# Optimization experiments

Hardware: AMD Instinct MI355X
Metric: run time of the kernel (lower is better)

## Reference

```python
import jax, jax.numpy as jnp
import numpy as np

N_POINTS = 10000
N_SHAPES = 100
N_RAYS = 4096
SH_COEFFS = 16  # (sh_degree+1)^2, degree 3


def sh_basis(d):
    """Degree-3 real SH basis. d: [B,3] normalized dirs -> [B,16]."""
    x, y, z = d[:, 0], d[:, 1], d[:, 2]
    one = jnp.ones_like(x)
    return jnp.stack([
        0.282095 * one,
        0.488603 * y, 0.488603 * z, 0.488603 * x,
        1.092548 * x * y, 1.092548 * y * z, 0.315392 * (3.0 * z * z - 1.0),
        1.092548 * x * z, 0.546274 * (x * x - y * y),
        0.590044 * y * (3.0 * x * x - y * y), 2.890611 * x * y * z,
        0.457046 * y * (5.0 * z * z - 1.0), 0.373176 * z * (5.0 * z * z - 3.0),
        0.457046 * x * (5.0 * z * z - 1.0), 1.445306 * z * (x * x - y * y),
        0.590044 * x * (x * x - 3.0 * y * y),
    ], axis=-1)


def setup_inputs() -> dict:
    key = jax.random.key(0)
    ks = jax.random.split(key, 7)
    return {
        "rays_o": jax.random.normal(ks[0], (N_RAYS, 3), jnp.float32),
        "rays_d": jax.random.normal(ks[1], (N_RAYS, 3), jnp.float32),
        "positions": jax.random.normal(ks[2], (N_POINTS, 3), jnp.float32),
        "shape_indices": jax.random.randint(ks[3], (N_POINTS,), 0, N_SHAPES, jnp.int32),
        "log_delta": jax.random.normal(ks[4], (N_SHAPES,), jnp.float32) * 0.1 - 1.0,
        "log_sigma": jax.random.normal(ks[5], (N_SHAPES,), jnp.float32) * 0.1,
        "raw_opacity": jax.random.uniform(ks[6], (N_POINTS,), jnp.float32, -0.1, 0.1),
        "sh_coeffs": jax.random.normal(jax.random.fold_in(key, 7), (N_POINTS, SH_COEFFS, 3), jnp.float32) * 0.1,
    }


def reference(rays_o, rays_d, positions, shape_indices, log_delta, log_sigma, raw_opacity, sh_coeffs):
    # normalize view directions (F.normalize)
    d_norm = rays_d / jnp.linalg.norm(rays_d, axis=-1, keepdims=True)

    opacity = jax.nn.sigmoid(raw_opacity)           # [N]
    point_delta = jnp.exp(log_delta)[shape_indices]  # [N]
    point_sigma = jnp.exp(log_sigma)[shape_indices]  # [N]

    # SH shading: colors [N, B, 3]
    sh = sh_basis(d_norm)                            # [B, 16]
    colors = jax.nn.sigmoid(jnp.einsum('nkc,bk->nbc', sh_coeffs, sh))

    # per point / per ray geometry
    rel = positions[:, None, :] - rays_o[None, :, :]   # [N, B, 3]
    dist = jnp.linalg.norm(rel, axis=2)                # [N, B]
    dirs = rel / (dist[..., None] + 1e-8)              # [N, B, 3]
    dot = jnp.sum(dirs * d_norm[None, :, :], axis=2)   # [N, B]

    contrib = (jnp.exp(-point_delta[:, None] * (1.0 - dot) ** 2)
               * point_sigma[:, None] * opacity[:, None] / (dist + 1e-6))  # [N, B]
    total = jnp.sum(contrib, axis=0, keepdims=True)
    w = contrib / (total + 1e-8)                       # [N, B]

    rgb = jnp.sum(colors * w[..., None], axis=0)       # [B, 3]
    depth = jnp.sum(dist * w, axis=0)[:, None]         # [B, 1]
    opac = jnp.broadcast_to(jnp.mean(opacity), (rgb.shape[0],))
    return rgb, depth, opac
```

## Files before the change

### kernel.cpp

```cpp
#include <hip/hip_runtime.h>
#include <hip/hip_bf16.h>

#define NPTS    10000
#define NRAYS   4096
#define PTILES  640
#define RTILES  256
#define RGROUPS 64
#define PCHUNKS 16
#define TPC     (PTILES / PCHUNKS)
#define ABLK    64
#define BBLK    160
#define LOG2E   1.44269504f

typedef float f4  __attribute__((ext_vector_type(4)));
typedef short s8v __attribute__((ext_vector_type(8)));

__device__ s8v   g_A[RTILES * 3 * 64];
__device__ s8v   g_B[PTILES * 5 * 64];
__device__ float g_acc[NRAYS * 5];
__device__ float g_oppart[BBLK];

__device__ __forceinline__ float fast_rcp(float x)  { return __builtin_amdgcn_rcpf(x); }
__device__ __forceinline__ float fast_exp2(float x) { return __builtin_amdgcn_exp2f(x); }
__device__ __forceinline__ float fast_sigmoid(float x) { return fast_rcp(1.0f + fast_exp2(-x * LOG2E)); }

__device__ __forceinline__ unsigned short bf16r(float x) {
    __hip_bfloat16 h = __float2bfloat16(x);
    return *reinterpret_cast<unsigned short*>(&h);
}
__device__ __forceinline__ float bf16f(unsigned short u) {
    return __uint_as_float((unsigned)u << 16);
}
__device__ __forceinline__ float bfhi(float x) { return bf16f(bf16r(x)); }

__device__ __forceinline__ s8v pk8(float a, float b, float c, float d,
                                   float e, float f, float g, float h) {
    s8v r;
    r[0] = (short)bf16r(a); r[1] = (short)bf16r(b);
    r[2] = (short)bf16r(c); r[3] = (short)bf16r(d);
    r[4] = (short)bf16r(e); r[5] = (short)bf16r(f);
    r[6] = (short)bf16r(g); r[7] = (short)bf16r(h);
    return r;
}

template <int CTRL>
__device__ __forceinline__ float dpp_step(float x) {
    return x + __int_as_float(
        __builtin_amdgcn_update_dpp(0, __float_as_int(x), CTRL, 0xf, 0xf, true));
}
__device__ __forceinline__ float rowsum15(float x) {
    x = dpp_step<0x111>(x);
    x = dpp_step<0x112>(x);
    x = dpp_step<0x114>(x);
    x = dpp_step<0x118>(x);
    return x;
}

__global__ __launch_bounds__(256) void setup(const float* __restrict__ ro,
                                             const float* __restrict__ rd,
                                             const float* __restrict__ pos,
                                             const int*   __restrict__ sidx,
                                             const float* __restrict__ log_delta,
                                             const float* __restrict__ log_sigma,
                                             const float* __restrict__ raw_op,
                                             const float* __restrict__ shc) {
    s8v zero8 = pk8(0, 0, 0, 0, 0, 0, 0, 0);
    if (blockIdx.x < ABLK) {
        int t = blockIdx.x * 256 + threadIdx.x;
        int rt = t >> 6, lane = t & 63, quad = lane >> 4;
        int r = rt * 16 + (lane & 15);
        if (quad == 0) {
            float* a = g_acc + (size_t)r * 5;
            a[0] = a[1] = a[2] = a[3] = a[4] = 0.0f;
        }
        float ox = ro[r * 3 + 0], oy = ro[r * 3 + 1], oz = ro[r * 3 + 2];
        float rdx = rd[r * 3 + 0], rdy = rd[r * 3 + 1], rdz = rd[r * 3 + 2];
        float inv = __builtin_amdgcn_rsqf(rdx * rdx + rdy * rdy + rdz * rdz);
        float x = rdx * inv, y = rdy * inv, z = rdz * inv;
        float oo = ox * ox + oy * oy + oz * oz;
        float od = ox * x + oy * y + oz * z;
        float ohx = bfhi(ox), olx = ox - ohx;
        float ohy = bfhi(oy), oly = oy - ohy;
        float ohz = bfhi(oz), olz = oz - ohz;
        float dhx = bfhi(x),  dlx = x - dhx;
        float dhy = bfhi(y),  dly = y - dhy;
        float dhz = bfhi(z),  dlz = z - dhz;
        float ooh = bfhi(oo), ool = oo - ooh;
        float odh = bfhi(od), odl = od - odh;
        float zz = z * z, xx = x * x, yy = y * y;
        float sh[16];
        sh[0]  = LOG2E * 0.282095f;
        sh[1]  = LOG2E * 0.488603f * y;
        sh[2]  = LOG2E * 0.488603f * z;
        sh[3]  = LOG2E * 0.488603f * x;
        sh[4]  = LOG2E * 1.092548f * x * y;
        sh[5]  = LOG2E * 1.092548f * y * z;
        sh[6]  = LOG2E * 0.315392f * (3.0f * zz - 1.0f);
        sh[7]  = LOG2E * 1.092548f * x * z;
        sh[8]  = LOG2E * 0.546274f * (xx - yy);
        sh[9]  = LOG2E * 0.590044f * y * (3.0f * xx - yy);
        sh[10] = LOG2E * 2.890611f * x * y * z;
        sh[11] = LOG2E * 0.457046f * y * (5.0f * zz - 1.0f);
        sh[12] = LOG2E * 0.373176f * z * (5.0f * zz - 3.0f);
        sh[13] = LOG2E * 0.457046f * x * (5.0f * zz - 1.0f);
        sh[14] = LOG2E * 1.445306f * z * (xx - yy);
        sh[15] = LOG2E * 0.590044f * x * (xx - 3.0f * yy);

        s8v A0 = quad == 0 ? pk8(1, 1, ooh, ool, ohx, ohy, ohz, ohx)
               : quad == 1 ? pk8(ohy, ohz, olx, oly, olz, 0, 0, 0) : zero8;
        s8v A1 = quad == 0 ? pk8(dhx, dhy, dhz, dhx, dhy, dhz, dlx, dly)
               : quad == 1 ? pk8(dlz, odh, odl, 0, 0, 0, 0, 0) : zero8;
        s8v A2 = quad == 0 ? pk8(sh[0], sh[1], sh[2], sh[3], sh[4], sh[5], sh[6], sh[7])
               : quad == 1 ? pk8(sh[8], sh[9], sh[10], sh[11], sh[12], sh[13], sh[14], sh[15]) : zero8;
        s8v* pa = g_A + (size_t)rt * 3 * 64 + lane;
        pa[0 * 64] = A0; pa[1 * 64] = A1; pa[2 * 64] = A2;
    } else {
        int bb = blockIdx.x - ABLK;
        int t  = bb * 256 + threadIdx.x;
        int pt = t >> 6, lane = t & 63, quad = lane >> 4;
        int n  = pt * 16 + (lane & 15);
        float px, py, pz, w1, L0, op = 0.0f;
        float C0[16], C1[16], C2[16];
        if (n < NPTS) {
            px = pos[n * 3 + 0]; py = pos[n * 3 + 1]; pz = pos[n * 3 + 2];
            int s = sidx[n];
            op = fast_sigmoid(raw_op[n]);
            w1 = -__expf(log_delta[s]) * LOG2E;
            float w0 = __expf(log_sigma[s]) * op;
            L0 = __log2f(w0);
            const float* c = shc + (size_t)n * 48;
#pragma unroll
            for (int k = 0; k < 16; ++k) {
                C0[k] = c[k * 3 + 0]; C1[k] = c[k * 3 + 1]; C2[k] = c[k * 3 + 2];
            }
        } else {
            px = py = pz = 1e3f; w1 = 0.0f; L0 = -100.0f;
#pragma unroll
            for (int k = 0; k < 16; ++k) { C0[k] = 0; C1[k] = 0; C2[k] = 0; }
        }
        float pp  = px * px + py * py + pz * pz;
        float phx = bfhi(px), plx = px - phx;
        float phy = bfhi(py), ply = py - phy;
        float phz = bfhi(pz), plz = pz - phz;
        float pph = bfhi(pp), ppl = pp - pph;
        float w1h = bfhi(w1), w1l = w1 - w1h;
        float L0h = bfhi(L0), L0l = L0 - L0h;

        s8v B0 = quad == 0 ? pk8(pph, ppl, 1, 1, -2 * phx, -2 * phy, -2 * phz, -2 * plx)
               : quad == 1 ? pk8(-2 * ply, -2 * plz, -2 * phx, -2 * phy, -2 * phz, w1h, w1l, 0) : zero8;
        s8v B1 = quad == 0 ? pk8(phx, phy, phz, plx, ply, plz, phx, phy)
               : quad == 1 ? pk8(phz, -1, -1, L0h, L0l, 0, 0, 0) : zero8;
        s8v B2 = quad == 0 ? pk8(C0[0], C0[1], C0[2], C0[3], C0[4], C0[5], C0[6], C0[7])
               : quad == 1 ? pk8(C0[8], C0[9], C0[10], C0[11], C0[12], C0[13], C0[14], C0[15]) : zero8;
        s8v B3 = quad == 0 ? pk8(C1[0], C1[1], C1[2], C1[3], C1[4], C1[5], C1[6], C1[7])
               : quad == 1 ? pk8(C1[8], C1[9], C1[10], C1[11], C1[12], C1[13], C1[14], C1[15]) : zero8;
        s8v B4 = quad == 0 ? pk8(C2[0], C2[1], C2[2], C2[3], C2[4], C2[5], C2[6], C2[7])
               : quad == 1 ? pk8(C2[8], C2[9], C2[10], C2[11], C2[12], C2[13], C2[14], C2[15]) : zero8;
        s8v* pb = g_B + (size_t)pt * 5 * 64 + lane;
        pb[0 * 64] = B0; pb[1 * 64] = B1; pb[2 * 64] = B2; pb[3 * 64] = B3;
        pb[4 * 64] = B4;

        __shared__ float blk;
        if (threadIdx.x == 0) blk = 0.0f;
        __syncthreads();
        float v = (quad == 0) ? op : 0.0f;
#pragma unroll
        for (int off = 32; off > 0; off >>= 1) v += __shfl_down(v, off, 64);
        if ((threadIdx.x & 63) == 0) atomicAdd(&blk, v);
        __syncthreads();
        if (threadIdx.x == 0) g_oppart[bb] = blk;
    }
}

__global__ __launch_bounds__(256, 3) void nerf_main() {
    int rg = blockIdx.x & (RGROUPS - 1);
    int pc = blockIdx.x / RGROUPS;
    int wv = threadIdx.x >> 6, lane = threadIdx.x & 63;
    int rt = rg * 4 + wv;
    int quad = lane >> 4;

    const s8v* pa = g_A + (size_t)rt * 3 * 64 + lane;
    s8v a0 = pa[0 * 64], a1 = pa[1 * 64], a2 = pa[2 * 64];
    short one_bf = (short)0x3F80;
    s8v a4 = {0, 0, 0, 0, 0, 0, 0, 0};
    s8v a5 = {0, 0, 0, 0, 0, 0, 0, 0};
    if (quad == 1) { a4[5] = one_bf; a4[6] = one_bf; a5[3] = one_bf; a5[4] = one_bf; }
    f4 z = {0.0f, 0.0f, 0.0f, 0.0f};

    float acc[5][4];
#pragma unroll
    for (int v = 0; v < 5; ++v)
#pragma unroll
        for (int i = 0; i < 4; ++i) acc[v][i] = 0.0f;

    const s8v* pb = g_B + (size_t)(pc * TPC) * 5 * 64 + lane;
#pragma unroll 1
    for (int ti = 0; ti < TPC; ++ti, pb += 5 * 64) {
        s8v b0 = pb[0 * 64], b1 = pb[1 * 64], b2 = pb[2 * 64], b3 = pb[3 * 64];
        s8v b4 = pb[4 * 64];
        f4 c0 = __builtin_amdgcn_mfma_f32_16x16x32_bf16(a0, b0, z, 0, 0, 0);
        f4 c1 = __builtin_amdgcn_mfma_f32_16x16x32_bf16(a1, b1, z, 0, 0, 0);
        f4 c2 = __builtin_amdgcn_mfma_f32_16x16x32_bf16(a2, b2, z, 0, 0, 0);
        f4 c3 = __builtin_amdgcn_mfma_f32_16x16x32_bf16(a2, b3, z, 0, 0, 0);
        f4 c4 = __builtin_amdgcn_mfma_f32_16x16x32_bf16(a2, b4, z, 0, 0, 0);
        f4 c5 = __builtin_amdgcn_mfma_f32_16x16x32_bf16(a4, b0, z, 0, 0, 0);
        f4 c6 = __builtin_amdgcn_mfma_f32_16x16x32_bf16(a5, b1, z, 0, 0, 0);
#pragma unroll
        for (int i = 0; i < 4; ++i) {
            float d2  = c0[i], pd = c1[i];
            float inv = __builtin_amdgcn_rsqf(d2);
            float t   = 1.0f - pd * inv;
            float arg = fmaf(c5[i] * t, t, c6[i]);
            float contrib = fast_exp2(arg) * inv;
            float dist = d2 * inv;
            float e0 = 1.0f + fast_exp2(-c2[i]);
            float e1 = 1.0f + fast_exp2(-c3[i]);
            float e2 = 1.0f + fast_exp2(-c4[i]);
            float P  = e0 * e1, Pa = P * e2;
            float CI = contrib * fast_rcp(Pa);
            acc[0][i] = fmaf(CI, e1 * e2, acc[0][i]);
            acc[1][i] = fmaf(CI, e0 * e2, acc[1][i]);
            acc[2][i] = fmaf(CI, P, acc[2][i]);
            acc[3][i] = fmaf(dist, contrib, acc[3][i]);
            acc[4][i] += contrib;
        }
    }

#pragma unroll
    for (int v = 0; v < 5; ++v)
#pragma unroll
        for (int i = 0; i < 4; ++i) acc[v][i] = rowsum15(acc[v][i]);
    if ((lane & 15) == 15) {
#pragma unroll
        for (int i = 0; i < 4; ++i) {
            float* ac = g_acc + (size_t)(rt * 16 + quad * 4 + i) * 5;
            atomicAdd(ac + 0, acc[0][i]);
            atomicAdd(ac + 1, acc[1][i]);
            atomicAdd(ac + 2, acc[2][i]);
            atomicAdd(ac + 3, acc[3][i]);
            atomicAdd(ac + 4, acc[4][i]);
        }
    }
}

__global__ void finalize(float* __restrict__ out) {
    int r = blockIdx.x * blockDim.x + threadIdx.x;
    if (r >= NRAYS) return;
    float opv = 0.0f;
    for (int i = 0; i < BBLK; ++i) opv += g_oppart[i];
    const float* a = g_acc + (size_t)r * 5;
    float inv = fast_rcp(a[4] + 1e-8f);
    out[r * 3 + 0]     = a[0] * inv;
    out[r * 3 + 1]     = a[1] * inv;
    out[r * 3 + 2]     = a[2] * inv;
    out[NRAYS * 3 + r] = a[3] * inv;
    out[NRAYS * 4 + r] = opv * (1.0f / NPTS);
}

extern "C" void kernel_launch(void* const* d_in, const int* in_sizes, int n_in,
                              void* d_out, int out_size, void* d_ws, size_t ws_size,
                              hipStream_t stream) {
    const float* rays_o    = (const float*)d_in[0];
    const float* rays_d    = (const float*)d_in[1];
    const float* positions = (const float*)d_in[2];
    const int*   sidx      = (const int*)d_in[3];
    const float* log_delta = (const float*)d_in[4];
    const float* log_sigma = (const float*)d_in[5];
    const float* raw_op    = (const float*)d_in[6];
    const float* shc       = (const float*)d_in[7];

    setup<<<ABLK + BBLK, 256, 0, stream>>>(
        rays_o, rays_d, positions, sidx, log_delta, log_sigma, raw_op, shc);
    nerf_main<<<RGROUPS * PCHUNKS, 256, 0, stream>>>();
    finalize<<<NRAYS / 256, 256, 0, stream>>>((float*)d_out);
}
```

Measured before the change: 128.9 us.

## Double-buffer point tiles in LDS with async global-to-LDS copies

Each block now cooperatively stages the shared point-tile B fragments into a double-buffered LDS array using global_load_lds, prefetching the next tile while computing the current one. Before this, each of the four waves loaded the same B data from global memory on its own, so the change removes that redundant traffic and hides load latency. In exchange it adds a block-wide barrier every iteration, some LDS use, and one padded extra tile so the final prefetch stays in bounds. The setup kernel also skips the coefficient loads on lanes whose values are unused.

```diff
diff --git a/kernel.cpp b/kernel.cpp
--- a/kernel.cpp
+++ b/kernel.cpp
@@ -16,7 +16,7 @@
 typedef short s8v __attribute__((ext_vector_type(8)));
 
 __device__ s8v   g_A[RTILES * 3 * 64];
-__device__ s8v   g_B[PTILES * 5 * 64];
+__device__ s8v   g_B[(PTILES + 1) * 5 * 64];
 __device__ float g_acc[NRAYS * 5];
 __device__ float g_oppart[BBLK];
 
@@ -43,6 +43,12 @@
     return r;
 }
 
+__device__ __forceinline__ void async_copy16(const void* g, void* l) {
+    __builtin_amdgcn_global_load_lds(
+        (const __attribute__((address_space(1))) void*)g,
+        (__attribute__((address_space(3))) void*)l, 16, 0, 0);
+}
+
 template <int CTRL>
 __device__ __forceinline__ float dpp_step(float x) {
     return x + __int_as_float(
@@ -64,7 +70,7 @@
                                              const float* __restrict__ log_sigma,
                                              const float* __restrict__ raw_op,
                                              const float* __restrict__ shc) {
-    s8v zero8 = pk8(0, 0, 0, 0, 0, 0, 0, 0);
+    s8v zero8 = {0, 0, 0, 0, 0, 0, 0, 0};
     if (blockIdx.x < ABLK) {
         int t = blockIdx.x * 256 + threadIdx.x;
         int rt = t >> 6, lane = t & 63, quad = lane >> 4;
@@ -119,9 +125,11 @@
         int t  = bb * 256 + threadIdx.x;
         int pt = t >> 6, lane = t & 63, quad = lane >> 4;
         int n  = pt * 16 + (lane & 15);
-        float px, py, pz, w1, L0, op = 0.0f;
+        float px = 1e3f, py = 1e3f, pz = 1e3f, w1 = 0.0f, L0 = -100.0f, op = 0.0f;
         float C0[16], C1[16], C2[16];
-        if (n < NPTS) {
+#pragma unroll
+        for (int k = 0; k < 16; ++k) { C0[k] = 0; C1[k] = 0; C2[k] = 0; }
+        if (n < NPTS && quad < 2) {
             px = pos[n * 3 + 0]; py = pos[n * 3 + 1]; pz = pos[n * 3 + 2];
             int s = sidx[n];
             op = fast_sigmoid(raw_op[n]);
@@ -133,10 +141,6 @@
             for (int k = 0; k < 16; ++k) {
                 C0[k] = c[k * 3 + 0]; C1[k] = c[k * 3 + 1]; C2[k] = c[k * 3 + 2];
             }
-        } else {
-            px = py = pz = 1e3f; w1 = 0.0f; L0 = -100.0f;
-#pragma unroll
-            for (int k = 0; k < 16; ++k) { C0[k] = 0; C1[k] = 0; C2[k] = 0; }
         }
         float pp  = px * px + py * py + pz * pz;
         float phx = bfhi(px), plx = px - phx;
@@ -173,6 +177,8 @@
 }
 
 __global__ __launch_bounds__(256, 3) void nerf_main() {
+    __shared__ s8v smB[2][5 * 64];
+
     int rg = blockIdx.x & (RGROUPS - 1);
     int pc = blockIdx.x / RGROUPS;
     int wv = threadIdx.x >> 6, lane = threadIdx.x & 63;
@@ -193,11 +199,22 @@
 #pragma unroll
         for (int i = 0; i < 4; ++i) acc[v][i] = 0.0f;
 
-    const s8v* pb = g_B + (size_t)(pc * TPC) * 5 * 64 + lane;
+    const s8v* gb = g_B + (size_t)(pc * TPC) * 5 * 64;
+
+    async_copy16(&gb[wv * 64 + lane], &smB[0][wv * 64]);
+    if (wv == 0) async_copy16(&gb[4 * 64 + lane], &smB[0][4 * 64]);
+    __syncthreads();
+
 #pragma unroll 1
-    for (int ti = 0; ti < TPC; ++ti, pb += 5 * 64) {
-        s8v b0 = pb[0 * 64], b1 = pb[1 * 64], b2 = pb[2 * 64], b3 = pb[3 * 64];
-        s8v b4 = pb[4 * 64];
+    for (int ti = 0; ti < TPC; ++ti) {
+        int cur = ti & 1, nxt = cur ^ 1;
+        const s8v* gt = gb + (size_t)(ti + 1) * 5 * 64;
+        async_copy16(&gt[wv * 64 + lane], &smB[nxt][wv * 64]);
+        if (wv == 0) async_copy16(&gt[4 * 64 + lane], &smB[nxt][4 * 64]);
+
+        const s8v* B = smB[cur];
+        s8v b0 = B[0 * 64 + lane], b1 = B[1 * 64 + lane], b2 = B[2 * 64 + lane];
+        s8v b3 = B[3 * 64 + lane], b4 = B[4 * 64 + lane];
         f4 c0 = __builtin_amdgcn_mfma_f32_16x16x32_bf16(a0, b0, z, 0, 0, 0);
         f4 c1 = __builtin_amdgcn_mfma_f32_16x16x32_bf16(a1, b1, z, 0, 0, 0);
         f4 c2 = __builtin_amdgcn_mfma_f32_16x16x32_bf16(a2, b2, z, 0, 0, 0);
@@ -224,6 +241,7 @@
             acc[3][i] = fmaf(dist, contrib, acc[3][i]);
             acc[4][i] += contrib;
         }
+        __syncthreads();
     }
 
 #pragma unroll
```

New measurement: 132.1 us. 1.02x slower.
